# Kernel tuning notes

Measured on AMD Instinct MI355X. Metric: run time of the kernel, lower is better.

## Reference

```python
import jax, jax.numpy as jnp
import numpy as np

UNITS = 4096
BATCH = 8192


def setup_inputs() -> dict:
    key = jax.random.key(0)
    kx, kw = jax.random.split(key)
    x = jax.random.normal(kx, (BATCH, UNITS), dtype=jnp.float32)
    # xavier_normal_ for square [units, units]: std = sqrt(2/(units+units)) = 1/sqrt(units)
    w = jax.random.normal(kw, (UNITS, UNITS), dtype=jnp.float32) * (1.0 / np.sqrt(UNITS))
    return {"x": x, "w": w}


def reference(x, w):
    # masked_w = w * eye(units); out = x @ masked_w
    units = w.shape[0]
    masked_w = w * jnp.eye(units, dtype=w.dtype)
    return x @ masked_w
```

## Files before the change

### kernel.cpp

```cpp
#include <hip/hip_runtime.h>

#define UNITS 4096
#define BATCH 8192

typedef float vf4 __attribute__((ext_vector_type(4)));

constexpr int TPB    = 256;
constexpr int NBLK   = 2048;
constexpr int STRIDE = TPB * NBLK;
constexpr int N4     = BATCH * UNITS / 4;
constexpr int ITERS  = N4 / STRIDE;

__global__ void __launch_bounds__(TPB)
diag_scale_kernel(const float* __restrict__ x,
                  const float* __restrict__ w,
                  float* __restrict__ out) {
    const vf4* __restrict__ x4 = (const vf4*)x;
    vf4* __restrict__ o4 = (vf4*)out;

    const int i0 = blockIdx.x * TPB + threadIdx.x;
    const int c  = i0 & (UNITS / 4 - 1);

    const size_t j0 = (size_t)(4 * c) * (UNITS + 1);
    vf4 dv;
    dv.x = w[j0];
    dv.y = w[j0 + (UNITS + 1)];
    dv.z = w[j0 + 2 * (UNITS + 1)];
    dv.w = w[j0 + 3 * (UNITS + 1)];

#pragma unroll
    for (int k = 0; k < ITERS; ++k) {
        const int i = i0 + k * STRIDE;
        vf4 xv = x4[i];
        vf4 ov = xv * dv;
        __builtin_nontemporal_store(ov, &o4[i]);
    }
}

extern "C" void kernel_launch(void* const* d_in, const int* in_sizes, int n_in,
                              void* d_out, int out_size, void* d_ws, size_t ws_size,
                              hipStream_t stream) {
    const float* x = (const float*)d_in[0];
    const float* w = (const float*)d_in[1];
    float* out = (float*)d_out;

    diag_scale_kernel<<<NBLK, TPB, 0, stream>>>(x, w, out);
}
```

Measured before the change: 53.09 us.

## Extract diagonal into workspace and launch one thread per vector element

Adds a small pre-kernel that gathers the diagonal of w into a contiguous workspace buffer. The scaling kernel then loads the diagonal with one vector load per thread and drops the grid-stride loop, launching one thread per float4 of x. The aim is to remove strided scalar gathers from the weight matrix. In exchange it adds a second kernel launch and many more blocks to schedule.

New measurement: 46.92 us. 11.6% less time.

```diff
diff --git a/kernel.cpp b/kernel.cpp
--- a/kernel.cpp
+++ b/kernel.cpp
@@ -5,36 +5,33 @@
 
 typedef float vf4 __attribute__((ext_vector_type(4)));
 
-constexpr int TPB    = 256;
-constexpr int NBLK   = 2048;
-constexpr int STRIDE = TPB * NBLK;
-constexpr int N4     = BATCH * UNITS / 4;
-constexpr int ITERS  = N4 / STRIDE;
+constexpr int TPB  = 256;
+constexpr int N4   = BATCH * UNITS / 4;
+constexpr int NBLK = N4 / TPB;
+
+__global__ void extract_diag_kernel(const float* __restrict__ w,
+                                    float* __restrict__ diag) {
+    int j = blockIdx.x * blockDim.x + threadIdx.x;
+    if (j < UNITS) {
+        diag[j] = w[(size_t)j * (UNITS + 1)];
+    }
+}
 
 __global__ void __launch_bounds__(TPB)
 diag_scale_kernel(const float* __restrict__ x,
-                  const float* __restrict__ w,
+                  const float* __restrict__ diag,
                   float* __restrict__ out) {
     const vf4* __restrict__ x4 = (const vf4*)x;
+    const vf4* __restrict__ d4 = (const vf4*)diag;
     vf4* __restrict__ o4 = (vf4*)out;
 
-    const int i0 = blockIdx.x * TPB + threadIdx.x;
-    const int c  = i0 & (UNITS / 4 - 1);
+    const int i = blockIdx.x * TPB + threadIdx.x;
+    const int c = i & (UNITS / 4 - 1);
 
-    const size_t j0 = (size_t)(4 * c) * (UNITS + 1);
-    vf4 dv;
-    dv.x = w[j0];
-    dv.y = w[j0 + (UNITS + 1)];
-    dv.z = w[j0 + 2 * (UNITS + 1)];
-    dv.w = w[j0 + 3 * (UNITS + 1)];
-
-#pragma unroll
-    for (int k = 0; k < ITERS; ++k) {
-        const int i = i0 + k * STRIDE;
-        vf4 xv = x4[i];
-        vf4 ov = xv * dv;
-        __builtin_nontemporal_store(ov, &o4[i]);
-    }
+    vf4 dv = d4[c];
+    vf4 xv = x4[i];
+    vf4 ov = xv * dv;
+    __builtin_nontemporal_store(ov, &o4[i]);
 }
 
 extern "C" void kernel_launch(void* const* d_in, const int* in_sizes, int n_in,
@@ -43,6 +40,8 @@
     const float* x = (const float*)d_in[0];
     const float* w = (const float*)d_in[1];
     float* out = (float*)d_out;
+    float* diag = (float*)d_ws;
 
-    diag_scale_kernel<<<NBLK, TPB, 0, stream>>>(x, w, out);
+    extract_diag_kernel<<<(UNITS + TPB - 1) / TPB, TPB, 0, stream>>>(w, diag);
+    diag_scale_kernel<<<NBLK, TPB, 0, stream>>>(x, diag, out);
 }
```
